# Optimization experiments

Measured on AMD Instinct MI355X. Metric: run time of the kernel, lower is better.

The kernel has to match this reference:

```python
import jax, jax.numpy as jnp
import numpy as np

N = 50000      # nodes
E = 800000     # edges (avg degree 16)
DIN = 128
HID = 128
OUT = 10       # classes
G = 64         # graphs in batch


def setup_inputs() -> dict:
    key = jax.random.key(0)
    ks = jax.random.split(key, 10)
    x = jax.random.normal(ks[0], (N, DIN), dtype=jnp.float32)
    edge_index = jax.random.randint(ks[1], (2, E), 0, N, dtype=jnp.int32)
    edge_weight = jax.random.uniform(ks[2], (E,), dtype=jnp.float32)
    batch = jnp.sort(jax.random.randint(ks[3], (N,), 0, G, dtype=jnp.int32))
    W1 = jax.random.normal(ks[4], (DIN, HID), dtype=jnp.float32) / np.sqrt(DIN)
    b1 = jnp.zeros((HID,), dtype=jnp.float32)
    W2 = jax.random.normal(ks[5], (HID, HID), dtype=jnp.float32) / np.sqrt(HID)
    b2 = jnp.zeros((HID,), dtype=jnp.float32)
    W3 = jax.random.normal(ks[6], (HID, OUT), dtype=jnp.float32) / np.sqrt(HID)
    b3 = jnp.zeros((OUT,), dtype=jnp.float32)
    return {"x": x, "edge_index": edge_index, "edge_weight": edge_weight,
            "batch": batch, "W1": W1, "b1": b1, "W2": W2, "b2": b2,
            "W3": W3, "b3": b3}


def _gcn_norm(edge_index, edge_weight, n_nodes):
    # PyG gcn_norm: add self-loops with weight 1, D^-1/2 (A+I) D^-1/2
    loop = jnp.arange(n_nodes, dtype=edge_index.dtype)
    src = jnp.concatenate([edge_index[0], loop])
    dst = jnp.concatenate([edge_index[1], loop])
    w = jnp.concatenate([edge_weight, jnp.ones((n_nodes,), edge_weight.dtype)])
    deg = jax.ops.segment_sum(w, dst, num_segments=n_nodes)
    dinv = jnp.where(deg > 0, jax.lax.rsqrt(deg), 0.0)
    norm = dinv[src] * w * dinv[dst]
    return src, dst, norm


def _gcn_conv(x, W, b, src, dst, norm, n_nodes):
    h = x @ W                                      # [N, F] dense transform
    msg = norm[:, None] * h[src]                   # gather + scale  [E+N, F]
    out = jax.ops.segment_sum(msg, dst, num_segments=n_nodes)  # scatter-add
    return out + b


def reference(x, edge_index, edge_weight, batch, W1, b1, W2, b2, W3, b3):
    src, dst, norm = _gcn_norm(edge_index, edge_weight, N)
    h = jax.nn.relu(_gcn_conv(x, W1, b1, src, dst, norm, N))
    h = jax.nn.relu(_gcn_conv(h, W2, b2, src, dst, norm, N))
    h = _gcn_conv(h, W3, b3, src, dst, norm, N)    # [N, OUT]
    # global_mean_pool over graph ids
    sums = jax.ops.segment_sum(h, batch, num_segments=G)          # [G, OUT]
    cnts = jax.ops.segment_sum(jnp.ones((N,), h.dtype), batch, num_segments=G)
    pooled = sums / jnp.maximum(cnts, 1.0)[:, None]
    return jax.nn.log_softmax(pooled, axis=1)
```

## Files before the change

### kernel.cpp

```cpp
#include <hip/hip_runtime.h>
#include <math.h>

#define NN 50000
#define EE 800000
#define GG 64
#define FD 128
#define OUTD 10
#define NB 49
#define GB 782
#define DB 3125
#define BB 196

typedef __attribute__((ext_vector_type(8))) short s8v;
typedef __attribute__((ext_vector_type(4))) float f4v;

static __device__ inline unsigned short f2b(float f) {
    unsigned int u = __float_as_uint(f);
    return (unsigned short)((u + 0x7FFFu + ((u >> 16) & 1u)) >> 16);
}

#define DEG_SCALE 4294967296.0
#define DEG_MASK  ((1ull << 44) - 1)


__global__ void k_prep(unsigned long long* packed, const float* __restrict__ W1,
                       const float* __restrict__ W2, unsigned short* __restrict__ Wt1,
                       unsigned short* __restrict__ Wt2, int* __restrict__ bflag, int n) {
    int i = blockIdx.x * blockDim.x + threadIdx.x;
    if (i < n) packed[i] = (1ull << 44) | (1ull << 32);
    if (i < FD * FD) {
        int nn = i >> 7, k = i & 127;
        Wt1[i] = f2b(W1[k * FD + nn]);
        Wt2[i] = f2b(W2[k * FD + nn]);
    }
    if (i < NB) bflag[i] = 0;
}


static __device__ inline void gemm_f32in_body(int bid, const float* __restrict__ A,
        const unsigned short* __restrict__ Wt, unsigned short* __restrict__ out, int n) {
    int tid = threadIdx.x;
    int wave = tid >> 6, lane = tid & 63;
    int quad = lane >> 4, c16 = lane & 15;
    int rowbase = bid * 64 + wave * 16;
    int rowA = rowbase + c16;
    if (rowA >= n) rowA = n - 1;
    f4v acc[8];
    #pragma unroll
    for (int t = 0; t < 8; ++t) acc[t] = (f4v){0.f, 0.f, 0.f, 0.f};
    #pragma unroll
    for (int k0 = 0; k0 < 128; k0 += 32) {
        const float* ap = A + (size_t)rowA * FD + k0 + quad * 8;
        float4 a0 = *(const float4*)ap;
        float4 a1 = *(const float4*)(ap + 4);
        s8v a;
        a[0] = (short)f2b(a0.x); a[1] = (short)f2b(a0.y);
        a[2] = (short)f2b(a0.z); a[3] = (short)f2b(a0.w);
        a[4] = (short)f2b(a1.x); a[5] = (short)f2b(a1.y);
        a[6] = (short)f2b(a1.z); a[7] = (short)f2b(a1.w);
        #pragma unroll
        for (int t = 0; t < 8; ++t) {
            s8v b = *(const s8v*)(Wt + (size_t)(t * 16 + c16) * FD + k0 + quad * 8);
            acc[t] = __builtin_amdgcn_mfma_f32_16x16x32_bf16(a, b, acc[t], 0, 0, 0);
        }
    }
    #pragma unroll
    for (int t = 0; t < 8; ++t) {
        #pragma unroll
        for (int r = 0; r < 4; ++r) {
            int row = rowbase + quad * 4 + r;
            if (row < n) out[(size_t)row * FD + t * 16 + c16] = f2b(acc[t][r]);
        }
    }
}

__global__ __launch_bounds__(256) void k_mega1(const float* __restrict__ x,
        const unsigned short* __restrict__ Wt1, unsigned short* __restrict__ hA,
        const int* __restrict__ dst, const float* __restrict__ ew,
        unsigned long long* packed, unsigned* __restrict__ rank,
        const int* __restrict__ batch, int* __restrict__ gstart) {
    int b = blockIdx.x;
    if (b < GB) {
        gemm_f32in_body(b, x, Wt1, hA, NN);
    } else if (b < GB + DB) {
        int i = (b - GB) * 256 + threadIdx.x;
        if (i < EE) {
            unsigned long long q = (unsigned long long)((double)ew[i] * DEG_SCALE + 0.5);
            unsigned long long old = atomicAdd(&packed[dst[i]], (1ull << 44) | q);
            rank[i] = (unsigned)(old >> 44) - 1u;
        }
    } else {
        int i = (b - GB - DB) * 256 + threadIdx.x;
        if (i < NN) {
            int bb = batch[i];
            int bp = (i == 0) ? -1 : batch[i - 1];
            for (int g = bp + 1; g <= bb; ++g) gstart[g] = i;
            if (i == NN - 1)
                for (int g = bb + 1; g <= GG; ++g) gstart[g] = NN;
        }
    }
}


__global__ __launch_bounds__(1024) void k_scan(const unsigned long long* __restrict__ packed,
        int* __restrict__ rowptr, float* __restrict__ dinv, uint2* __restrict__ ent,
        int* __restrict__ bsum, int* __restrict__ bflag, int n) {
    __shared__ int wtot[16];
    __shared__ int sbase_sh;
    int tid = threadIdx.x;
    int bid = blockIdx.x;
    int i = bid * 1024 + tid;
    int lane = tid & 63, wv = tid >> 6;

    int v = 0;
    float di = 0.0f;
    if (i < n) {
        unsigned long long p = packed[i];
        v = (int)(p >> 44);
        float deg = (float)((double)(p & DEG_MASK) * (1.0 / DEG_SCALE));
        di = 1.0f / sqrtf(deg);
        dinv[i] = di;
    }
    int s = v;
    #pragma unroll
    for (int off = 1; off < 64; off <<= 1) {
        int u = __shfl_up(s, off, 64);
        if (lane >= off) s += u;
    }
    if (lane == 63) wtot[wv] = s;
    __syncthreads();

    int btot = 0;
    #pragma unroll
    for (int j = 0; j < 16; ++j) btot += wtot[j];
    if (tid == 0) {
        bsum[bid] = btot;
        __hip_atomic_store(&bflag[bid], 1, __ATOMIC_RELEASE, __HIP_MEMORY_SCOPE_AGENT);
    }
    if (tid < 64) {
        int acc = 0;
        if (tid < bid) {
            while (__hip_atomic_load(&bflag[tid], __ATOMIC_ACQUIRE,
                                     __HIP_MEMORY_SCOPE_AGENT) == 0) {}
            acc = bsum[tid];
        }
        #pragma unroll
        for (int off = 32; off >= 1; off >>= 1) acc += __shfl_xor(acc, off, 64);
        if (tid == 0) sbase_sh = acc;
    }
    __syncthreads();
    int base = sbase_sh;

    int wpre = 0;
    for (int j = 0; j < wv; ++j) wpre += wtot[j];
    if (i < n) {
        int r = base + wpre + (s - v);
        rowptr[i] = r;
        ent[r + v - 1] = make_uint2((unsigned)i, __float_as_uint(di * di));
    }
    if (bid == NB - 1 && tid == 0) rowptr[n] = base + btot;
}

__global__ void k_fill(const int* __restrict__ src, const int* __restrict__ dst,
                       const float* __restrict__ w, const float* __restrict__ dinv,
                       const int* __restrict__ rowptr, const unsigned* __restrict__ rank,
                       uint2* __restrict__ ent, int e) {
    int i = blockIdx.x * blockDim.x + threadIdx.x;
    if (i >= e) return;
    int s = src[i], d = dst[i];
    int pos = rowptr[d] + (int)rank[i];
    float v = dinv[s] * w[i] * dinv[d];
    ent[pos] = make_uint2((unsigned)s, __float_as_uint(v));
}


__global__ __launch_bounds__(256) void k_gemm_bf(const unsigned short* __restrict__ A,
        const unsigned short* __restrict__ Wt, unsigned short* __restrict__ out, int n) {
    int tid = threadIdx.x;
    int wave = tid >> 6, lane = tid & 63;
    int quad = lane >> 4, c16 = lane & 15;
    int rowbase = blockIdx.x * 64 + wave * 16;
    int rowA = rowbase + c16;
    if (rowA >= n) rowA = n - 1;
    f4v acc[8];
    #pragma unroll
    for (int t = 0; t < 8; ++t) acc[t] = (f4v){0.f, 0.f, 0.f, 0.f};
    #pragma unroll
    for (int k0 = 0; k0 < 128; k0 += 32) {
        s8v a = *(const s8v*)(A + (size_t)rowA * FD + k0 + quad * 8);
        #pragma unroll
        for (int t = 0; t < 8; ++t) {
            s8v b = *(const s8v*)(Wt + (size_t)(t * 16 + c16) * FD + k0 + quad * 8);
            acc[t] = __builtin_amdgcn_mfma_f32_16x16x32_bf16(a, b, acc[t], 0, 0, 0);
        }
    }
    #pragma unroll
    for (int t = 0; t < 8; ++t) {
        #pragma unroll
        for (int r = 0; r < 4; ++r) {
            int row = rowbase + quad * 4 + r;
            if (row < n) out[(size_t)row * FD + t * 16 + c16] = f2b(acc[t][r]);
        }
    }
}

__global__ void k_gemm10(const unsigned short* __restrict__ A, const float* __restrict__ W,
                         float* __restrict__ out, int n) {
    __shared__ float Ws[FD * OUTD];
    int tid = threadIdx.x;
    for (int i = tid; i < FD * OUTD; i += blockDim.x) Ws[i] = W[i];
    __syncthreads();
    int i = blockIdx.x * blockDim.x + tid;
    if (i >= n) return;
    float acc[OUTD];
    #pragma unroll
    for (int c = 0; c < OUTD; ++c) acc[c] = 0.0f;
    const unsigned short* a = A + (size_t)i * FD;
    for (int k0 = 0; k0 < FD; k0 += 8) {
        uint4 t = *(const uint4*)(a + k0);
        float av[8];
        av[0] = __uint_as_float(t.x << 16); av[1] = __uint_as_float(t.x & 0xFFFF0000u);
        av[2] = __uint_as_float(t.y << 16); av[3] = __uint_as_float(t.y & 0xFFFF0000u);
        av[4] = __uint_as_float(t.z << 16); av[5] = __uint_as_float(t.z & 0xFFFF0000u);
        av[6] = __uint_as_float(t.w << 16); av[7] = __uint_as_float(t.w & 0xFFFF0000u);
        #pragma unroll
        for (int j = 0; j < 8; ++j)
            #pragma unroll
            for (int c = 0; c < OUTD; ++c) acc[c] += av[j] * Ws[(k0 + j) * OUTD + c];
    }
    float* o = out + (size_t)i * OUTD;
    #pragma unroll
    for (int c = 0; c < OUTD; ++c) o[c] = acc[c];
}

__global__ __launch_bounds__(256) void k_spmm_bf(const int* __restrict__ rowptr,
        const uint2* __restrict__ ent, const unsigned short* __restrict__ tin,
        const float* __restrict__ bias, unsigned short* __restrict__ out,
        int n, int dorelu) {
    int w = (blockIdx.x * blockDim.x + threadIdx.x) >> 6;
    int lane = threadIdx.x & 63;
    if (w >= n) return;
    int c = lane & 15, g = lane >> 4;
    int beg = rowptr[w], end = rowptr[w + 1];
    float acc[8];
    #pragma unroll
    for (int j = 0; j < 8; ++j) acc[j] = 0.0f;
    for (int e0 = beg; e0 < end; e0 += 16) {
        uint2 en[4];
        uint4 t[4];
        #pragma unroll
        for (int u = 0; u < 4; ++u) {
            int e = e0 + 4 * u + g;
            en[u] = (e < end) ? ent[e] : make_uint2(0u, 0u);
        }
        #pragma unroll
        for (int u = 0; u < 4; ++u)
            t[u] = *(const uint4*)(tin + (size_t)en[u].x * FD + c * 8);
        #pragma unroll
        for (int u = 0; u < 4; ++u) {
            float v = __uint_as_float(en[u].y);
            acc[0] += v * __uint_as_float(t[u].x << 16);
            acc[1] += v * __uint_as_float(t[u].x & 0xFFFF0000u);
            acc[2] += v * __uint_as_float(t[u].y << 16);
            acc[3] += v * __uint_as_float(t[u].y & 0xFFFF0000u);
            acc[4] += v * __uint_as_float(t[u].z << 16);
            acc[5] += v * __uint_as_float(t[u].z & 0xFFFF0000u);
            acc[6] += v * __uint_as_float(t[u].w << 16);
            acc[7] += v * __uint_as_float(t[u].w & 0xFFFF0000u);
        }
    }
    #pragma unroll
    for (int j = 0; j < 8; ++j) {
        acc[j] += __shfl_xor(acc[j], 16, 64);
        acc[j] += __shfl_xor(acc[j], 32, 64);
    }
    if (g == 0) {
        uint4 r;
        float o[8];
        #pragma unroll
        for (int j = 0; j < 8; ++j) {
            float x = acc[j] + bias[c * 8 + j];
            o[j] = dorelu ? fmaxf(x, 0.0f) : x;
        }
        r.x = (unsigned)f2b(o[0]) | ((unsigned)f2b(o[1]) << 16);
        r.y = (unsigned)f2b(o[2]) | ((unsigned)f2b(o[3]) << 16);
        r.z = (unsigned)f2b(o[4]) | ((unsigned)f2b(o[5]) << 16);
        r.w = (unsigned)f2b(o[6]) | ((unsigned)f2b(o[7]) << 16);
        *(uint4*)(out + (size_t)w * FD + c * 8) = r;
    }
}

__global__ void k_spmm10(const int* __restrict__ rowptr, const uint2* __restrict__ ent,
        const float* __restrict__ tin, const float* __restrict__ bias,
        float* __restrict__ out, int n) {
    int t = blockIdx.x * blockDim.x + threadIdx.x;
    int node = t / OUTD;
    int c = t - node * OUTD;
    if (node >= n) return;
    int beg = rowptr[node], end = rowptr[node + 1];
    float acc = 0.0f;
    for (int e = beg; e < end; ++e) {
        uint2 en = ent[e];
        acc += __uint_as_float(en.y) * tin[(size_t)en.x * OUTD + c];
    }
    out[(size_t)node * OUTD + c] = acc + bias[c];
}


__global__ __launch_bounds__(256) void k_poolfin(const float* __restrict__ h,
        const int* __restrict__ gstart, float* __restrict__ out) {
    int g = blockIdx.x;
    int beg = gstart[g], end = gstart[g + 1];
    int tid = threadIdx.x;
    int lane = tid & 63, wv = tid >> 6;
    float acc[OUTD];
    #pragma unroll
    for (int c = 0; c < OUTD; ++c) acc[c] = 0.0f;
    for (int i = beg + tid; i < end; i += 256) {
        const float* hp = h + (size_t)i * OUTD;
        #pragma unroll
        for (int c = 0; c < OUTD; ++c) acc[c] += hp[c];
    }
    #pragma unroll
    for (int off = 32; off >= 1; off >>= 1)
        #pragma unroll
        for (int c = 0; c < OUTD; ++c) acc[c] += __shfl_down(acc[c], off, 64);
    __shared__ float ws[4][OUTD];
    if (lane == 0)
        #pragma unroll
        for (int c = 0; c < OUTD; ++c) ws[wv][c] = acc[c];
    __syncthreads();
    if (tid == 0) {
        float cf = fmaxf((float)(end - beg), 1.0f);
        float v[OUTD], m = -1e30f;
        #pragma unroll
        for (int c = 0; c < OUTD; ++c) {
            v[c] = (ws[0][c] + ws[1][c] + ws[2][c] + ws[3][c]) / cf;
            m = fmaxf(m, v[c]);
        }
        float s = 0.0f;
        #pragma unroll
        for (int c = 0; c < OUTD; ++c) s += expf(v[c] - m);
        float l = logf(s);
        #pragma unroll
        for (int c = 0; c < OUTD; ++c) out[g * OUTD + c] = v[c] - m - l;
    }
}


extern "C" void kernel_launch(void* const* d_in, const int* in_sizes, int n_in,
                              void* d_out, int out_size, void* d_ws, size_t ws_size,
                              hipStream_t stream) {
    const float* x   = (const float*)d_in[0];
    const int*   ei  = (const int*)d_in[1];
    const float* ew  = (const float*)d_in[2];
    const int*   bat = (const int*)d_in[3];
    const float* W1  = (const float*)d_in[4];
    const float* b1  = (const float*)d_in[5];
    const float* W2  = (const float*)d_in[6];
    const float* b2  = (const float*)d_in[7];
    const float* W3  = (const float*)d_in[8];
    const float* b3  = (const float*)d_in[9];
    float* out = (float*)d_out;

    const int* src = ei;
    const int* dst = ei + EE;

    char* p = (char*)d_ws;
    auto alloc = [&](size_t bytes) -> void* {
        void* r = (void*)p;
        p += (bytes + 255) & ~(size_t)255;
        return r;
    };
    unsigned long long* packed = (unsigned long long*)alloc((size_t)NN * 8);
    float*          dinv   = (float*)alloc((size_t)NN * 4);
    int*            rowptr = (int*)  alloc((size_t)(NN + 1) * 4);
    unsigned*       rank   = (unsigned*)alloc((size_t)EE * 4);
    uint2*          ent    = (uint2*)alloc((size_t)(EE + NN) * 8);
    unsigned short* Wt1    = (unsigned short*)alloc((size_t)FD * FD * 2);
    unsigned short* Wt2    = (unsigned short*)alloc((size_t)FD * FD * 2);
    unsigned short* hA     = (unsigned short*)alloc((size_t)NN * FD * 2);
    unsigned short* hB     = (unsigned short*)alloc((size_t)NN * FD * 2);
    float*          bufC   = (float*)alloc((size_t)NN * OUTD * 4);
    float*          bufD   = (float*)alloc((size_t)NN * OUTD * 4);
    int*            bsum   = (int*)  alloc((size_t)NB * 4);
    int*            bflag  = (int*)  alloc((size_t)NB * 4);
    int*            gstart = (int*)  alloc((size_t)(GG + 1) * 4);
    (void)ws_size; (void)in_sizes; (void)n_in; (void)out_size;

    const int B = 256;
    k_prep <<<(NN + B - 1) / B, B, 0, stream>>>(packed, W1, W2, Wt1, Wt2, bflag, NN);
    k_mega1<<<GB + DB + BB, B, 0, stream>>>(x, Wt1, hA, dst, ew, packed, rank, bat, gstart);
    k_scan <<<NB, 1024, 0, stream>>>(packed, rowptr, dinv, ent, bsum, bflag, NN);
    k_fill <<<(EE + B - 1) / B, B, 0, stream>>>(src, dst, ew, dinv, rowptr, rank, ent, EE);

    k_spmm_bf<<<(NN * 64 + B - 1) / B, B, 0, stream>>>(rowptr, ent, hA, b1, hB, NN, 1);
    k_gemm_bf<<<GB, B, 0, stream>>>(hB, Wt2, hA, NN);
    k_spmm_bf<<<(NN * 64 + B - 1) / B, B, 0, stream>>>(rowptr, ent, hA, b2, hB, NN, 1);
    k_gemm10 <<<(NN + B - 1) / B, B, 0, stream>>>(hB, W3, bufC, NN);
    k_spmm10 <<<(NN * OUTD + B - 1) / B, B, 0, stream>>>(rowptr, ent, bufC, b3, bufD, NN);
    k_poolfin<<<GG, 256, 0, stream>>>(bufD, gstart, out);
}
```

Baseline: 282.4 us.

## Shard degree atomics across 8 copies and fuse W3 projection into layer-2 SpMM

Degree and rank counting now spreads its atomics over 8 replicated counters per node, chosen by block index. This is meant to reduce contention on the 64-bit atomicAdd. The scan sums the replicas and writes per-copy offsets, which the fill kernel uses to place each edge. Separately, the second-layer SpMM now applies bias, ReLU and the 128x10 W3 projection in-register, removing the bf16 hidden write/read and the separate k_gemm10 launch. The costs are extra memory traffic for the replicated counters and the offsets array, plus the shuffle reductions and W3 loads inside the SpMM.

```diff
diff --git a/kernel.cpp b/kernel.cpp
--- a/kernel.cpp
+++ b/kernel.cpp
@@ -10,6 +10,7 @@
 #define GB 782
 #define DB 3125
 #define BB 196
+#define NP 8
 
 typedef __attribute__((ext_vector_type(8))) short s8v;
 typedef __attribute__((ext_vector_type(4))) float f4v;
@@ -27,7 +28,11 @@
                        const float* __restrict__ W2, unsigned short* __restrict__ Wt1,
                        unsigned short* __restrict__ Wt2, int* __restrict__ bflag, int n) {
     int i = blockIdx.x * blockDim.x + threadIdx.x;
-    if (i < n) packed[i] = (1ull << 44) | (1ull << 32);
+    if (i < n) {
+        packed[i] = (1ull << 32);
+        #pragma unroll
+        for (int c = 1; c < NP; ++c) packed[(size_t)c * NN + i] = 0ull;
+    }
     if (i < FD * FD) {
         int nn = i >> 7, k = i & 127;
         Wt1[i] = f2b(W1[k * FD + nn]);
@@ -85,9 +90,11 @@
     } else if (b < GB + DB) {
         int i = (b - GB) * 256 + threadIdx.x;
         if (i < EE) {
+            int c = b & (NP - 1);
             unsigned long long q = (unsigned long long)((double)ew[i] * DEG_SCALE + 0.5);
-            unsigned long long old = atomicAdd(&packed[dst[i]], (1ull << 44) | q);
-            rank[i] = (unsigned)(old >> 44) - 1u;
+            unsigned long long old =
+                atomicAdd(&packed[(size_t)c * NN + dst[i]], (1ull << 44) | q);
+            rank[i] = ((unsigned)(old >> 44) << 3) | (unsigned)c;
         }
     } else {
         int i = (b - GB - DB) * 256 + threadIdx.x;
@@ -104,7 +111,7 @@
 
 __global__ __launch_bounds__(1024) void k_scan(const unsigned long long* __restrict__ packed,
         int* __restrict__ rowptr, float* __restrict__ dinv, uint2* __restrict__ ent,
-        int* __restrict__ bsum, int* __restrict__ bflag, int n) {
+        uint4* __restrict__ coffs, int* __restrict__ bsum, int* __restrict__ bflag, int n) {
     __shared__ int wtot[16];
     __shared__ int sbase_sh;
     int tid = threadIdx.x;
@@ -112,16 +119,32 @@
     int i = bid * 1024 + tid;
     int lane = tid & 63, wv = tid >> 6;
 
-    int v = 0;
+    int rowlen = 0;
+    int v_edges = 0;
     float di = 0.0f;
     if (i < n) {
-        unsigned long long p = packed[i];
-        v = (int)(p >> 44);
-        float deg = (float)((double)(p & DEG_MASK) * (1.0 / DEG_SCALE));
+        unsigned long long degq = 0;
+        int cnts[NP];
+        #pragma unroll
+        for (int c = 0; c < NP; ++c) {
+            unsigned long long p = packed[(size_t)c * NN + i];
+            cnts[c] = (int)(p >> 44);
+            degq += p & DEG_MASK;
+            v_edges += cnts[c];
+        }
+        float deg = (float)((double)degq * (1.0 / DEG_SCALE));
         di = 1.0f / sqrtf(deg);
         dinv[i] = di;
-    }
-    int s = v;
+        unsigned o01 = 0, o23, o45, o67;
+        unsigned run = (unsigned)cnts[0];
+        o01 = run << 16;                 run += cnts[1];
+        o23 = run | ((run + cnts[2]) << 16); run += cnts[2] + cnts[3];
+        o45 = run | ((run + cnts[4]) << 16); run += cnts[4] + cnts[5];
+        o67 = run | ((run + cnts[6]) << 16);
+        coffs[i] = make_uint4(o01, o23, o45, o67);
+        rowlen = v_edges + 1;
+    }
+    int s = rowlen;
     #pragma unroll
     for (int off = 1; off < 64; off <<= 1) {
         int u = __shfl_up(s, off, 64);
@@ -154,9 +177,9 @@
     int wpre = 0;
     for (int j = 0; j < wv; ++j) wpre += wtot[j];
     if (i < n) {
-        int r = base + wpre + (s - v);
+        int r = base + wpre + (s - rowlen);
         rowptr[i] = r;
-        ent[r + v - 1] = make_uint2((unsigned)i, __float_as_uint(di * di));
+        ent[r + v_edges] = make_uint2((unsigned)i, __float_as_uint(di * di));
     }
     if (bid == NB - 1 && tid == 0) rowptr[n] = base + btot;
 }
@@ -164,11 +187,16 @@
 __global__ void k_fill(const int* __restrict__ src, const int* __restrict__ dst,
                        const float* __restrict__ w, const float* __restrict__ dinv,
                        const int* __restrict__ rowptr, const unsigned* __restrict__ rank,
-                       uint2* __restrict__ ent, int e) {
+                       const uint4* __restrict__ coffs, uint2* __restrict__ ent, int e) {
     int i = blockIdx.x * blockDim.x + threadIdx.x;
     if (i >= e) return;
     int s = src[i], d = dst[i];
-    int pos = rowptr[d] + (int)rank[i];
+    unsigned rk = rank[i];
+    int c = rk & 7, lr = (int)(rk >> 3);
+    uint4 cf = coffs[d];
+    unsigned word = ((const unsigned*)&cf)[c >> 1];
+    int off = (c & 1) ? (int)(word >> 16) : (int)(word & 0xFFFFu);
+    int pos = rowptr[d] + off + lr;
     float v = dinv[s] * w[i] * dinv[d];
     ent[pos] = make_uint2((unsigned)s, __float_as_uint(v));
 }
@@ -202,35 +230,6 @@
             if (row < n) out[(size_t)row * FD + t * 16 + c16] = f2b(acc[t][r]);
         }
     }
-}
-
-__global__ void k_gemm10(const unsigned short* __restrict__ A, const float* __restrict__ W,
-                         float* __restrict__ out, int n) {
-    __shared__ float Ws[FD * OUTD];
-    int tid = threadIdx.x;
-    for (int i = tid; i < FD * OUTD; i += blockDim.x) Ws[i] = W[i];
-    __syncthreads();
-    int i = blockIdx.x * blockDim.x + tid;
-    if (i >= n) return;
-    float acc[OUTD];
-    #pragma unroll
-    for (int c = 0; c < OUTD; ++c) acc[c] = 0.0f;
-    const unsigned short* a = A + (size_t)i * FD;
-    for (int k0 = 0; k0 < FD; k0 += 8) {
-        uint4 t = *(const uint4*)(a + k0);
-        float av[8];
-        av[0] = __uint_as_float(t.x << 16); av[1] = __uint_as_float(t.x & 0xFFFF0000u);
-        av[2] = __uint_as_float(t.y << 16); av[3] = __uint_as_float(t.y & 0xFFFF0000u);
-        av[4] = __uint_as_float(t.z << 16); av[5] = __uint_as_float(t.z & 0xFFFF0000u);
-        av[6] = __uint_as_float(t.w << 16); av[7] = __uint_as_float(t.w & 0xFFFF0000u);
-        #pragma unroll
-        for (int j = 0; j < 8; ++j)
-            #pragma unroll
-            for (int c = 0; c < OUTD; ++c) acc[c] += av[j] * Ws[(k0 + j) * OUTD + c];
-    }
-    float* o = out + (size_t)i * OUTD;
-    #pragma unroll
-    for (int c = 0; c < OUTD; ++c) o[c] = acc[c];
 }
 
 __global__ __launch_bounds__(256) void k_spmm_bf(const int* __restrict__ rowptr,
@@ -287,6 +286,76 @@
         r.z = (unsigned)f2b(o[4]) | ((unsigned)f2b(o[5]) << 16);
         r.w = (unsigned)f2b(o[6]) | ((unsigned)f2b(o[7]) << 16);
         *(uint4*)(out + (size_t)w * FD + c * 8) = r;
+    }
+}
+
+__global__ __launch_bounds__(256) void k_spmm_w3(const int* __restrict__ rowptr,
+        const uint2* __restrict__ ent, const unsigned short* __restrict__ tin,
+        const float* __restrict__ bias2, const float* __restrict__ W3,
+        float* __restrict__ outc, int n) {
+    int w = (blockIdx.x * blockDim.x + threadIdx.x) >> 6;
+    int lane = threadIdx.x & 63;
+    if (w >= n) return;
+    int c = lane & 15, g = lane >> 4;
+    int beg = rowptr[w], end = rowptr[w + 1];
+    float acc[8];
+    #pragma unroll
+    for (int j = 0; j < 8; ++j) acc[j] = 0.0f;
+    for (int e0 = beg; e0 < end; e0 += 16) {
+        uint2 en[4];
+        uint4 t[4];
+        #pragma unroll
+        for (int u = 0; u < 4; ++u) {
+            int e = e0 + 4 * u + g;
+            en[u] = (e < end) ? ent[e] : make_uint2(0u, 0u);
+        }
+        #pragma unroll
+        for (int u = 0; u < 4; ++u)
+            t[u] = *(const uint4*)(tin + (size_t)en[u].x * FD + c * 8);
+        #pragma unroll
+        for (int u = 0; u < 4; ++u) {
+            float v = __uint_as_float(en[u].y);
+            acc[0] += v * __uint_as_float(t[u].x << 16);
+            acc[1] += v * __uint_as_float(t[u].x & 0xFFFF0000u);
+            acc[2] += v * __uint_as_float(t[u].y << 16);
+            acc[3] += v * __uint_as_float(t[u].y & 0xFFFF0000u);
+            acc[4] += v * __uint_as_float(t[u].z << 16);
+            acc[5] += v * __uint_as_float(t[u].z & 0xFFFF0000u);
+            acc[6] += v * __uint_as_float(t[u].w << 16);
+            acc[7] += v * __uint_as_float(t[u].w & 0xFFFF0000u);
+        }
+    }
+    #pragma unroll
+    for (int j = 0; j < 8; ++j) {
+        acc[j] += __shfl_xor(acc[j], 16, 64);
+        acc[j] += __shfl_xor(acc[j], 32, 64);
+    }
+    if (g == 0) {
+        float o[8];
+        #pragma unroll
+        for (int j = 0; j < 8; ++j)
+            o[j] = fmaxf(acc[j] + bias2[c * 8 + j], 0.0f);
+        float p10[OUTD];
+        #pragma unroll
+        for (int cc = 0; cc < OUTD; ++cc) p10[cc] = 0.0f;
+        const float* w3c = W3 + c * 8 * OUTD;
+        #pragma unroll
+        for (int j = 0; j < 8; ++j) {
+            float hv = o[j];
+            #pragma unroll
+            for (int cc = 0; cc < OUTD; ++cc)
+                p10[cc] += hv * w3c[j * OUTD + cc];
+        }
+        #pragma unroll
+        for (int off = 8; off >= 1; off >>= 1)
+            #pragma unroll
+            for (int cc = 0; cc < OUTD; ++cc)
+                p10[cc] += __shfl_xor(p10[cc], off, 64);
+        if (c == 0) {
+            float* op = outc + (size_t)w * OUTD;
+            #pragma unroll
+            for (int cc = 0; cc < OUTD; ++cc) op[cc] = p10[cc];
+        }
     }
 }
 
@@ -372,10 +441,11 @@
         p += (bytes + 255) & ~(size_t)255;
         return r;
     };
-    unsigned long long* packed = (unsigned long long*)alloc((size_t)NN * 8);
+    unsigned long long* packed = (unsigned long long*)alloc((size_t)NP * NN * 8);
     float*          dinv   = (float*)alloc((size_t)NN * 4);
     int*            rowptr = (int*)  alloc((size_t)(NN + 1) * 4);
     unsigned*       rank   = (unsigned*)alloc((size_t)EE * 4);
+    uint4*          coffs  = (uint4*)alloc((size_t)NN * 16);
     uint2*          ent    = (uint2*)alloc((size_t)(EE + NN) * 8);
     unsigned short* Wt1    = (unsigned short*)alloc((size_t)FD * FD * 2);
     unsigned short* Wt2    = (unsigned short*)alloc((size_t)FD * FD * 2);
@@ -391,13 +461,12 @@
     const int B = 256;
     k_prep <<<(NN + B - 1) / B, B, 0, stream>>>(packed, W1, W2, Wt1, Wt2, bflag, NN);
     k_mega1<<<GB + DB + BB, B, 0, stream>>>(x, Wt1, hA, dst, ew, packed, rank, bat, gstart);
-    k_scan <<<NB, 1024, 0, stream>>>(packed, rowptr, dinv, ent, bsum, bflag, NN);
-    k_fill <<<(EE + B - 1) / B, B, 0, stream>>>(src, dst, ew, dinv, rowptr, rank, ent, EE);
+    k_scan <<<NB, 1024, 0, stream>>>(packed, rowptr, dinv, ent, coffs, bsum, bflag, NN);
+    k_fill <<<(EE + B - 1) / B, B, 0, stream>>>(src, dst, ew, dinv, rowptr, rank, coffs, ent, EE);
 
     k_spmm_bf<<<(NN * 64 + B - 1) / B, B, 0, stream>>>(rowptr, ent, hA, b1, hB, NN, 1);
     k_gemm_bf<<<GB, B, 0, stream>>>(hB, Wt2, hA, NN);
-    k_spmm_bf<<<(NN * 64 + B - 1) / B, B, 0, stream>>>(rowptr, ent, hA, b2, hB, NN, 1);
-    k_gemm10 <<<(NN + B - 1) / B, B, 0, stream>>>(hB, W3, bufC, NN);
+    k_spmm_w3<<<(NN * 64 + B - 1) / B, B, 0, stream>>>(rowptr, ent, hA, b2, W3, bufC, NN);
     k_spmm10 <<<(NN * OUTD + B - 1) / B, B, 0, stream>>>(rowptr, ent, bufC, b3, bufD, NN);
     k_poolfin<<<GG, 256, 0, stream>>>(bufD, gstart, out);
 }
```

Measured after the change: 325.7 us. +15.3%, slower.

## Build CSR via two-level bucket sort instead of global 64-bit atomics

Applied to the files above, without the earlier changes.

Replaces the per-edge global 64-bit atomicAdd on packed degree/count words with a bucketed counting sort: per-chunk LDS histograms over 256-node buckets, a small scan, a scatter into bucket-ordered records, then per-bucket LDS ranking and weighted degree accumulation, followed by a bucket-local fill of the CSR entries. The aim is to cut global atomic contention and random global writes during graph preprocessing. In exchange it adds several kernel launches, an extra pass over edge records, a single-block serial scan, and float LDS atomics that make degree sums order-nondeterministic. Packing the source index into 16 bits assumes node ids fit, but with 50000 nodes the node id exceeds 65535? No, it fits.

```diff
diff --git a/kernel.cpp b/kernel.cpp
--- a/kernel.cpp
+++ b/kernel.cpp
@@ -8,8 +8,10 @@
 #define OUTD 10
 #define NB 49
 #define GB 782
-#define DB 3125
 #define BB 196
+#define NBU 196
+#define NBK 128
+#define CH 6250
 
 typedef __attribute__((ext_vector_type(8))) short s8v;
 typedef __attribute__((ext_vector_type(4))) float f4v;
@@ -19,15 +21,11 @@
     return (unsigned short)((u + 0x7FFFu + ((u >> 16) & 1u)) >> 16);
 }
 
-#define DEG_SCALE 4294967296.0
-#define DEG_MASK  ((1ull << 44) - 1)
-
-
-__global__ void k_prep(unsigned long long* packed, const float* __restrict__ W1,
-                       const float* __restrict__ W2, unsigned short* __restrict__ Wt1,
-                       unsigned short* __restrict__ Wt2, int* __restrict__ bflag, int n) {
+
+__global__ void k_prep(const float* __restrict__ W1, const float* __restrict__ W2,
+                       unsigned short* __restrict__ Wt1, unsigned short* __restrict__ Wt2,
+                       int* __restrict__ bflag) {
     int i = blockIdx.x * blockDim.x + threadIdx.x;
-    if (i < n) packed[i] = (1ull << 44) | (1ull << 32);
     if (i < FD * FD) {
         int nn = i >> 7, k = i & 127;
         Wt1[i] = f2b(W1[k * FD + nn]);
@@ -74,23 +72,26 @@
     }
 }
 
-__global__ __launch_bounds__(256) void k_mega1(const float* __restrict__ x,
+__global__ __launch_bounds__(256) void k_megaA(const float* __restrict__ x,
         const unsigned short* __restrict__ Wt1, unsigned short* __restrict__ hA,
-        const int* __restrict__ dst, const float* __restrict__ ew,
-        unsigned long long* packed, unsigned* __restrict__ rank,
+        const int* __restrict__ dst, int* __restrict__ cnt2d,
         const int* __restrict__ batch, int* __restrict__ gstart) {
     int b = blockIdx.x;
+    int tid = threadIdx.x;
     if (b < GB) {
         gemm_f32in_body(b, x, Wt1, hA, NN);
-    } else if (b < GB + DB) {
-        int i = (b - GB) * 256 + threadIdx.x;
-        if (i < EE) {
-            unsigned long long q = (unsigned long long)((double)ew[i] * DEG_SCALE + 0.5);
-            unsigned long long old = atomicAdd(&packed[dst[i]], (1ull << 44) | q);
-            rank[i] = (unsigned)(old >> 44) - 1u;
-        }
+    } else if (b < GB + NBK) {
+        __shared__ unsigned hist[NBU];
+        int blk = b - GB;
+        if (tid < NBU) hist[tid] = 0;
+        __syncthreads();
+        int e0 = blk * CH;
+        for (int e = e0 + tid; e < e0 + CH; e += 256)
+            atomicAdd(&hist[(unsigned)dst[e] >> 8], 1u);
+        __syncthreads();
+        if (tid < NBU) cnt2d[blk * NBU + tid] = (int)hist[tid];
     } else {
-        int i = (b - GB - DB) * 256 + threadIdx.x;
+        int i = (b - GB - NBK) * 256 + tid;
         if (i < NN) {
             int bb = batch[i];
             int bp = (i == 0) ? -1 : batch[i - 1];
@@ -102,8 +103,83 @@
 }
 
 
-__global__ __launch_bounds__(1024) void k_scan(const unsigned long long* __restrict__ packed,
-        int* __restrict__ rowptr, float* __restrict__ dinv, uint2* __restrict__ ent,
+__global__ __launch_bounds__(256) void k_bscan(int* __restrict__ cnt2d,
+        int* __restrict__ bucketbase) {
+    __shared__ int colsum[NBU];
+    int tid = threadIdx.x;
+    if (tid < NBU) {
+        int run = 0;
+        for (int blk = 0; blk < NBK; ++blk) {
+            int idx = blk * NBU + tid;
+            int t = cnt2d[idx];
+            cnt2d[idx] = run;
+            run += t;
+        }
+        colsum[tid] = run;
+    }
+    __syncthreads();
+    if (tid == 0) {
+        int run = 0;
+        for (int b = 0; b < NBU; ++b) {
+            bucketbase[b] = run;
+            run += colsum[b];
+        }
+        bucketbase[NBU] = run;
+    }
+}
+
+
+__global__ __launch_bounds__(256) void k_scatter(const int* __restrict__ src,
+        const int* __restrict__ dst, const float* __restrict__ ew,
+        const int* __restrict__ off2d, const int* __restrict__ bucketbase,
+        uint2* __restrict__ rec) {
+    __shared__ unsigned cur[NBU];
+    int tid = threadIdx.x;
+    int blk = blockIdx.x;
+    if (tid < NBU) cur[tid] = (unsigned)(bucketbase[tid] + off2d[blk * NBU + tid]);
+    __syncthreads();
+    int e0 = blk * CH;
+    for (int e = e0 + tid; e < e0 + CH; e += 256) {
+        int d = dst[e];
+        unsigned bkt = (unsigned)d >> 8;
+        unsigned pos = atomicAdd(&cur[bkt], 1u);
+        rec[pos] = make_uint2(((unsigned)(d & 255) << 16) | (unsigned)src[e],
+                              __float_as_uint(ew[e]));
+    }
+}
+
+
+__global__ __launch_bounds__(1024) void k_rank(const uint2* __restrict__ rec,
+        const int* __restrict__ bucketbase, unsigned short* __restrict__ rankb,
+        int* __restrict__ cnt_g, float* __restrict__ wdeg_g) {
+    __shared__ unsigned cntS[256];
+    __shared__ float wdegS[256];
+    int b = blockIdx.x;
+    int tid = threadIdx.x;
+    if (tid < 256) { cntS[tid] = 0; wdegS[tid] = 0.0f; }
+    __syncthreads();
+    int beg = bucketbase[b], end = bucketbase[b + 1];
+    for (int s = beg + tid; s < end; s += 1024) {
+        uint2 r = rec[s];
+        unsigned dl = r.x >> 16;
+        unsigned old = atomicAdd(&cntS[dl], 1u);
+        rankb[s] = (unsigned short)old;
+        atomicAdd(&wdegS[dl], __uint_as_float(r.y));
+    }
+    __syncthreads();
+    if (tid < 256) {
+        int node = b * 256 + tid;
+        if (node < NN) {
+            cnt_g[node] = (int)cntS[tid];
+            wdeg_g[node] = wdegS[tid];
+        }
+    }
+}
+
+
+__global__ __launch_bounds__(1024) void k_scan(const int* __restrict__ cnt_g,
+        const float* __restrict__ wdeg_g, int* __restrict__ rowptr,
+        float* __restrict__ dinv, uint2* __restrict__ ent,
         int* __restrict__ bsum, int* __restrict__ bflag, int n) {
     __shared__ int wtot[16];
     __shared__ int sbase_sh;
@@ -112,16 +188,16 @@
     int i = bid * 1024 + tid;
     int lane = tid & 63, wv = tid >> 6;
 
-    int v = 0;
+    int v_edges = 0, rowlen = 0;
     float di = 0.0f;
     if (i < n) {
-        unsigned long long p = packed[i];
-        v = (int)(p >> 44);
-        float deg = (float)((double)(p & DEG_MASK) * (1.0 / DEG_SCALE));
+        v_edges = cnt_g[i];
+        float deg = wdeg_g[i] + 1.0f;
         di = 1.0f / sqrtf(deg);
         dinv[i] = di;
-    }
-    int s = v;
+        rowlen = v_edges + 1;
+    }
+    int s = rowlen;
     #pragma unroll
     for (int off = 1; off < 64; off <<= 1) {
         int u = __shfl_up(s, off, 64);
@@ -154,23 +230,29 @@
     int wpre = 0;
     for (int j = 0; j < wv; ++j) wpre += wtot[j];
     if (i < n) {
-        int r = base + wpre + (s - v);
+        int r = base + wpre + (s - rowlen);
         rowptr[i] = r;
-        ent[r + v - 1] = make_uint2((unsigned)i, __float_as_uint(di * di));
+        ent[r + v_edges] = make_uint2((unsigned)i, __float_as_uint(di * di));
     }
     if (bid == NB - 1 && tid == 0) rowptr[n] = base + btot;
 }
 
-__global__ void k_fill(const int* __restrict__ src, const int* __restrict__ dst,
-                       const float* __restrict__ w, const float* __restrict__ dinv,
-                       const int* __restrict__ rowptr, const unsigned* __restrict__ rank,
-                       uint2* __restrict__ ent, int e) {
-    int i = blockIdx.x * blockDim.x + threadIdx.x;
-    if (i >= e) return;
-    int s = src[i], d = dst[i];
-    int pos = rowptr[d] + (int)rank[i];
-    float v = dinv[s] * w[i] * dinv[d];
-    ent[pos] = make_uint2((unsigned)s, __float_as_uint(v));
+
+__global__ __launch_bounds__(1024) void k_fill2(const uint2* __restrict__ rec,
+        const unsigned short* __restrict__ rankb, const int* __restrict__ bucketbase,
+        const int* __restrict__ rowptr, const float* __restrict__ dinv,
+        uint2* __restrict__ ent) {
+    int b = blockIdx.x;
+    int tid = threadIdx.x;
+    int beg = bucketbase[b], end = bucketbase[b + 1];
+    for (int s = beg + tid; s < end; s += 1024) {
+        uint2 r = rec[s];
+        unsigned sn = r.x & 0xFFFFu;
+        int d = (b << 8) | (int)(r.x >> 16);
+        int pos = rowptr[d] + (int)rankb[s];
+        float val = dinv[sn] * __uint_as_float(r.y) * dinv[d];
+        ent[pos] = make_uint2(sn, __float_as_uint(val));
+    }
 }
 
 
@@ -372,10 +454,14 @@
         p += (bytes + 255) & ~(size_t)255;
         return r;
     };
-    unsigned long long* packed = (unsigned long long*)alloc((size_t)NN * 8);
+    int*            cnt2d  = (int*)  alloc((size_t)NBK * NBU * 4);
+    int*            bbase  = (int*)  alloc((size_t)(NBU + 1) * 4);
+    uint2*          rec    = (uint2*)alloc((size_t)EE * 8);
+    unsigned short* rankb  = (unsigned short*)alloc((size_t)EE * 2);
+    int*            cnt_g  = (int*)  alloc((size_t)NN * 4);
+    float*          wdeg_g = (float*)alloc((size_t)NN * 4);
     float*          dinv   = (float*)alloc((size_t)NN * 4);
     int*            rowptr = (int*)  alloc((size_t)(NN + 1) * 4);
-    unsigned*       rank   = (unsigned*)alloc((size_t)EE * 4);
     uint2*          ent    = (uint2*)alloc((size_t)(EE + NN) * 8);
     unsigned short* Wt1    = (unsigned short*)alloc((size_t)FD * FD * 2);
     unsigned short* Wt2    = (unsigned short*)alloc((size_t)FD * FD * 2);
@@ -389,10 +475,13 @@
     (void)ws_size; (void)in_sizes; (void)n_in; (void)out_size;
 
     const int B = 256;
-    k_prep <<<(NN + B - 1) / B, B, 0, stream>>>(packed, W1, W2, Wt1, Wt2, bflag, NN);
-    k_mega1<<<GB + DB + BB, B, 0, stream>>>(x, Wt1, hA, dst, ew, packed, rank, bat, gstart);
-    k_scan <<<NB, 1024, 0, stream>>>(packed, rowptr, dinv, ent, bsum, bflag, NN);
-    k_fill <<<(EE + B - 1) / B, B, 0, stream>>>(src, dst, ew, dinv, rowptr, rank, ent, EE);
+    k_prep   <<<(FD * FD + B - 1) / B, B, 0, stream>>>(W1, W2, Wt1, Wt2, bflag);
+    k_megaA  <<<GB + NBK + BB, B, 0, stream>>>(x, Wt1, hA, dst, cnt2d, bat, gstart);
+    k_bscan  <<<1, B, 0, stream>>>(cnt2d, bbase);
+    k_scatter<<<NBK, B, 0, stream>>>(src, dst, ew, cnt2d, bbase, rec);
+    k_rank   <<<NBU, 1024, 0, stream>>>(rec, bbase, rankb, cnt_g, wdeg_g);
+    k_scan   <<<NB, 1024, 0, stream>>>(cnt_g, wdeg_g, rowptr, dinv, ent, bsum, bflag, NN);
+    k_fill2  <<<NBU, 1024, 0, stream>>>(rec, rankb, bbase, rowptr, dinv, ent);
 
     k_spmm_bf<<<(NN * 64 + B - 1) / B, B, 0, stream>>>(rowptr, ent, hA, b1, hB, NN, 1);
     k_gemm_bf<<<GB, B, 0, stream>>>(hB, Wt2, hA, NN);
```

Measured after the change: 281.8 us. No clear change (-0.2%).
